# Optimization experiments

Hardware: AMD Instinct MI355X
Metric: run time of the kernel (lower is better)

## Reference

```python
import math
import jax, jax.numpy as jnp
import numpy as np


def _pairwise_sqdist(x, y):
    # x: [N, d], y: [M, d] -> [N, M]
    x2 = jnp.sum(x * x, axis=-1)[:, None]
    y2 = jnp.sum(y * y, axis=-1)[None, :]
    return jnp.maximum(x2 + y2 - 2.0 * (x @ y.T), 0.0)


def setup_inputs() -> dict:
    key = jax.random.key(0)
    k1, k2 = jax.random.split(key)
    N, M, D = 8192, 8192, 2
    base_points = jax.random.normal(k1, (N, D), dtype=jnp.float32)
    target_points = jax.random.normal(k2, (M, D), dtype=jnp.float32)
    log_sigma = jnp.asarray(math.log(0.1), dtype=jnp.float32)
    log_scale = jnp.zeros((D,), dtype=jnp.float32)
    return {
        "base_points": base_points,
        "target_points": target_points,
        "log_sigma": log_sigma,
        "log_scale": log_scale,
    }


def reference(base_points, target_points, log_sigma, log_scale):
    # learn_scale=True: anisotropic per-coordinate scaling
    scale = jnp.exp(log_scale)
    base = base_points * scale
    target = target_points * scale

    # uniform node weights (use_weight_net=False)
    N = base.shape[0]
    M = target.shape[0]
    w_base = jnp.full((N,), 1.0 / N, dtype=base.dtype)
    w_target = jnp.full((M,), 1.0 / M, dtype=target.dtype)

    # center=True: subtract weighted centroid of each cloud
    base = base - jnp.sum(w_base[:, None] * base, axis=0, keepdims=True)
    target = target - jnp.sum(w_target[:, None] * target, axis=0, keepdims=True)

    sigma = jnp.exp(log_sigma)
    inv2s2 = 1.0 / (2.0 * sigma * sigma)

    k_bb = jnp.exp(-_pairwise_sqdist(base, base) * inv2s2)      # [N, N]
    k_tt = jnp.exp(-_pairwise_sqdist(target, target) * inv2s2)  # [M, M]
    k_bt = jnp.exp(-_pairwise_sqdist(base, target) * inv2s2)    # [N, M]

    term_bb = w_base @ (k_bb @ w_base)
    term_tt = w_target @ (k_tt @ w_target)
    term_bt = w_base @ (k_bt @ w_target)
    loss = term_bb + term_tt - 2.0 * term_bt
    return loss
```

## Files before the change

kernel.cpp:

```cpp
#include <hip/hip_runtime.h>


#define BLOCK 256
#define NT_CROSS 1024
#define NT_TOT   2080
#define LOG2E 1.4426950408889634f

typedef float v2f __attribute__((ext_vector_type(2)));

struct Prep { float f0, f1, sh0, sh1; };

__device__ __forceinline__ float fexp2(float x) {
    return __builtin_amdgcn_exp2f(x);
}

__global__ __launch_bounds__(1024) void prep_kernel(
    const float* __restrict__ base, const float* __restrict__ target,
    const float* __restrict__ log_sigma, const float* __restrict__ log_scale,
    int N, int M, Prep* __restrict__ pp, double* __restrict__ slots)
{
    __shared__ double mred[16][4];
    const int tid = threadIdx.x;
    if (tid < 64) slots[tid] = 0.0;

    double sbx = 0, sby = 0, stx = 0, sty = 0;
    const float4* b4 = (const float4*)base;
    const float4* t4 = (const float4*)target;
    for (int i = tid; i < (N >> 1); i += 1024) {
        float4 v = b4[i];
        sbx += (double)v.x + (double)v.z;
        sby += (double)v.y + (double)v.w;
    }
    for (int i = tid; i < (M >> 1); i += 1024) {
        float4 v = t4[i];
        stx += (double)v.x + (double)v.z;
        sty += (double)v.y + (double)v.w;
    }
    for (int off = 32; off; off >>= 1) {
        sbx += __shfl_down(sbx, off); sby += __shfl_down(sby, off);
        stx += __shfl_down(stx, off); sty += __shfl_down(sty, off);
    }
    if ((tid & 63) == 0) {
        mred[tid >> 6][0] = sbx; mred[tid >> 6][1] = sby;
        mred[tid >> 6][2] = stx; mred[tid >> 6][3] = sty;
    }
    __syncthreads();
    if (tid == 0) {
        double b0 = 0, b1 = 0, t0 = 0, t1 = 0;
        for (int k = 0; k < 16; ++k) {
            b0 += mred[k][0]; b1 += mred[k][1];
            t0 += mred[k][2]; t1 += mred[k][3];
        }
        float s0 = expf(log_scale[0]);
        float s1 = expf(log_scale[1]);
        float sigma = expf(log_sigma[0]);
        float inv2s2 = 1.0f / (2.0f * sigma * sigma);
        float sq = sqrtf(inv2s2 * LOG2E);
        float f0 = s0 * sq, f1 = s1 * sq;
        pp->f0 = f0; pp->f1 = f1;
        pp->sh0 = (float)(b0 / (double)N - t0 / (double)M) * f0;
        pp->sh1 = (float)(b1 / (double)N - t1 / (double)M) * f1;
    }
}

__global__ __launch_bounds__(BLOCK, 8) void mmd_main(
    const float* __restrict__ base, const float* __restrict__ target,
    int N, int M, const Prep* __restrict__ pp, double* __restrict__ slots)
{
    __shared__ __align__(16) float tbx[256];
    __shared__ __align__(16) float tby[256];
    __shared__ __align__(16) float tbc[256];
    __shared__ double wredd[4];

    const int tid = threadIdx.x;
    const int t   = blockIdx.x;
    const Prep p = *pp;
    const float2* base2   = (const float2*)base;
    const float2* target2 = (const float2*)target;

    const double wNN = 1.0 / ((double)N * (double)N);
    const double wMM = 1.0 / ((double)M * (double)M);
    const double wNM = -2.0 / ((double)N * (double)M);

    int ib, jb, term;
    bool diag;
    const float2* A2;
    const float2* B2;
    double wt;
    float shx = 0.f, shy = 0.f;
    if (t < NT_CROSS) {
        ib = t >> 5; jb = t & 31;
        A2 = base2; B2 = target2;
        wt = wNM; diag = false; term = 2;
        shx = p.sh0; shy = p.sh1;
    } else {
        const int u = t - NT_CROSS;
        term = (u >= 528) ? 1 : 0;
        const int v = u - term * 528;
        int r = (int)((65.0f - sqrtf(4225.0f - 8.0f * (float)v)) * 0.5f);
        r = min(max(r, 0), 31);
        while (r > 0 && (r * (65 - r)) / 2 > v) --r;
        while (r < 31 && ((r + 1) * (64 - r)) / 2 <= v) ++r;
        ib = r;
        jb = r + (v - (r * (65 - r)) / 2);
        diag = (jb == ib);
        A2 = term ? target2 : base2;  B2 = A2;
        wt = 2.0 * (term ? wMM : wNN);
    }
    const int i0 = ib * 256, j0 = jb * 256;

    {
        float2 b = B2[j0 + tid];
        float bx = b.x * p.f0, by = b.y * p.f1;
        tbx[tid] = bx;
        tby[tid] = by;
        tbc[tid] = -fmaf(bx, bx, by * by);
    }
    __syncthreads();

    const int r0 = i0 + (tid & 127);
    const int js = (tid >> 7) * 128;

    float ax2s[2], ay2s[2], A0s[2];
#pragma unroll
    for (int k = 0; k < 2; ++k) {
        float2 a = A2[r0 + 128 * k];
        float ax = fmaf(a.x, p.f0, -shx);
        float ay = fmaf(a.y, p.f1, -shy);
        ax2s[k] = ax + ax;
        ay2s[k] = ay + ay;
        A0s[k]  = -fmaf(ax, ax, ay * ay);
    }

    const float4* bx4 = (const float4*)(tbx + js);
    const float4* by4 = (const float4*)(tby + js);
    const float4* c4  = (const float4*)(tbc + js);

    double result;
    if (!diag) {
        v2f s00 = {0.f, 0.f}, s01 = {0.f, 0.f};
        v2f s10 = {0.f, 0.f}, s11 = {0.f, 0.f};
#pragma unroll 4
        for (int q = 0; q < 32; ++q) {
            float4 BX = bx4[q];
            float4 BY = by4[q];
            float4 C  = c4[q];
            v2f bxa = { BX.x, BX.y }, bxb = { BX.z, BX.w };
            v2f bya = { BY.x, BY.y }, byb = { BY.z, BY.w };
            v2f ca  = { C.x,  C.y  }, cb  = { C.z,  C.w  };
            {
                v2f A0v = { A0s[0], A0s[0] };
                v2f axv = { ax2s[0], ax2s[0] };
                v2f ayv = { ay2s[0], ay2s[0] };
                v2f ea = axv * bxa + (ayv * bya + (ca + A0v));
                v2f eb = axv * bxb + (ayv * byb + (cb + A0v));
                s00 += (v2f){ fexp2(ea.x), fexp2(ea.y) };
                s01 += (v2f){ fexp2(eb.x), fexp2(eb.y) };
            }
            {
                v2f A0v = { A0s[1], A0s[1] };
                v2f axv = { ax2s[1], ax2s[1] };
                v2f ayv = { ay2s[1], ay2s[1] };
                v2f ea = axv * bxa + (ayv * bya + (ca + A0v));
                v2f eb = axv * bxb + (ayv * byb + (cb + A0v));
                s10 += (v2f){ fexp2(ea.x), fexp2(ea.y) };
                s11 += (v2f){ fexp2(eb.x), fexp2(eb.y) };
            }
        }
        v2f st0 = s00 + s01;
        v2f st1 = s10 + s11;
        result = wt * ((double)(st0.x + st0.y) + (double)(st1.x + st1.y));
    } else {
        float sge = 0.f, sgt = 0.f;
        const int jbase = j0 + js;
#pragma unroll 2
        for (int q = 0; q < 32; ++q) {
            float4 BX = bx4[q];
            float4 BY = by4[q];
            float4 C  = c4[q];
            const int j = jbase + 4 * q;
#pragma unroll
            for (int k = 0; k < 2; ++k) {
                const int row = r0 + 128 * k;
                float e0 = fmaf(ax2s[k], BX.x, fmaf(ay2s[k], BY.x, C.x + A0s[k]));
                float e1 = fmaf(ax2s[k], BX.y, fmaf(ay2s[k], BY.y, C.y + A0s[k]));
                float e2 = fmaf(ax2s[k], BX.z, fmaf(ay2s[k], BY.z, C.z + A0s[k]));
                float e3 = fmaf(ax2s[k], BX.w, fmaf(ay2s[k], BY.w, C.w + A0s[k]));
                float v0 = fexp2(e0), v1 = fexp2(e1);
                float v2 = fexp2(e2), v3 = fexp2(e3);
                sge += (j + 0 >= row) ? v0 : 0.f;  sgt += (j + 0 > row) ? v0 : 0.f;
                sge += (j + 1 >= row) ? v1 : 0.f;  sgt += (j + 1 > row) ? v1 : 0.f;
                sge += (j + 2 >= row) ? v2 : 0.f;  sgt += (j + 2 > row) ? v2 : 0.f;
                sge += (j + 3 >= row) ? v3 : 0.f;  sgt += (j + 3 > row) ? v3 : 0.f;
            }
        }
        result = (term ? wMM : wNN) * (double)(sge + sgt);
    }

    for (int off = 32; off; off >>= 1) result += __shfl_down(result, off);
    if ((tid & 63) == 0) wredd[tid >> 6] = result;
    __syncthreads();
    if (tid == 0) {
        double s = wredd[0] + wredd[1] + wredd[2] + wredd[3];
        atomicAdd(&slots[t & 63], s);
    }
}

__global__ void final_kernel(const double* __restrict__ slots,
                             float* __restrict__ out)
{
    const int tid = threadIdx.x;
    double s = slots[tid];
    for (int off = 32; off; off >>= 1) s += __shfl_down(s, off);
    if (tid == 0) out[0] = (float)s;
}

extern "C" void kernel_launch(void* const* d_in, const int* in_sizes, int n_in,
                              void* d_out, int out_size, void* d_ws, size_t ws_size,
                              hipStream_t stream)
{
    const float* base      = (const float*)d_in[0];
    const float* target    = (const float*)d_in[1];
    const float* log_sigma = (const float*)d_in[2];
    const float* log_scale = (const float*)d_in[3];
    float* out = (float*)d_out;

    int N = in_sizes[0] / 2;
    int M = in_sizes[1] / 2;

    Prep*   pp    = (Prep*)d_ws;
    double* slots = (double*)((char*)d_ws + 64);

    prep_kernel<<<1, 1024, 0, stream>>>(base, target, log_sigma, log_scale,
                                        N, M, pp, slots);
    mmd_main<<<NT_TOT, BLOCK, 0, stream>>>(base, target, N, M, pp, slots);
    final_kernel<<<1, 64, 0, stream>>>(slots, out);
}
```

Baseline: 90.53 us.

## Bucket-sort points by x and skip Gaussian tile quads beyond cutoff

Adds a counting-sort kernel that bins scaled, centred points by x into 512 buckets and writes them out as SoA arrays with precomputed squared norms. The main kernel then computes per-wave row x-ranges and per-quad column x-ranges, and skips four-column groups whose x-distance exceeds a cutoff, where the kernel value falls below about 2^-40. Block indices are permuted to balance the now-uneven work, and the rows handled by each thread become adjacent pairs. This trades an extra serial two-block sort kernel and branch divergence for skipping most exp evaluations. Skipped terms are treated as zero, which approximates the exact result only to within a tiny error.

```diff
diff --git a/kernel.cpp b/kernel.cpp
--- a/kernel.cpp
+++ b/kernel.cpp
@@ -4,7 +4,11 @@
 #define BLOCK 256
 #define NT_CROSS 1024
 #define NT_TOT   2080
-#define LOG2E 1.4426950408889634f
+#define LOG2E  1.4426950408889634f
+#define NBUCK  512
+#define BXMIN  (-64.0f)
+#define BSCALE 4.0f
+#define CUT    6.32455532f
 
 typedef float v2f __attribute__((ext_vector_type(2)));
 
@@ -63,20 +67,74 @@
     }
 }
 
+__global__ __launch_bounds__(1024) void sort_kernel(
+    const float* __restrict__ base, const float* __restrict__ target,
+    int N, int M, const Prep* __restrict__ pp,
+    float* __restrict__ xsB, float* __restrict__ ysB, float* __restrict__ csB,
+    float* __restrict__ xsT, float* __restrict__ ysT, float* __restrict__ csT)
+{
+    __shared__ unsigned hist[NBUCK];
+    __shared__ unsigned pref[NBUCK];
+    __shared__ unsigned cnt[NBUCK];
+    const int tid = threadIdx.x;
+    const Prep p = *pp;
+    const bool isB = (blockIdx.x == 0);
+    const float2* src = (const float2*)(isB ? base : target);
+    const int n = isB ? N : M;
+    float* xs = isB ? xsB : xsT;
+    float* ys = isB ? ysB : ysT;
+    float* cs = isB ? csB : csT;
+    const float shx = isB ? p.sh0 : 0.f;
+    const float shy = isB ? p.sh1 : 0.f;
+
+    for (int i = tid; i < NBUCK; i += 1024) { hist[i] = 0u; cnt[i] = 0u; }
+    __syncthreads();
+    for (int i = tid; i < n; i += 1024) {
+        float2 a = src[i];
+        float x = fmaf(a.x, p.f0, -shx);
+        int b = (int)((x - BXMIN) * BSCALE);
+        b = min(max(b, 0), NBUCK - 1);
+        atomicAdd(&hist[b], 1u);
+    }
+    __syncthreads();
+    if (tid < NBUCK) pref[tid] = hist[tid];
+    __syncthreads();
+    for (int off = 1; off < NBUCK; off <<= 1) {
+        unsigned v = 0u;
+        if (tid < NBUCK && tid >= off) v = pref[tid - off];
+        __syncthreads();
+        if (tid < NBUCK) pref[tid] += v;
+        __syncthreads();
+    }
+    for (int i = tid; i < n; i += 1024) {
+        float2 a = src[i];
+        float x = fmaf(a.x, p.f0, -shx);
+        float y = fmaf(a.y, p.f1, -shy);
+        int b = (int)((x - BXMIN) * BSCALE);
+        b = min(max(b, 0), NBUCK - 1);
+        unsigned pos = pref[b] - hist[b] + atomicAdd(&cnt[b], 1u);
+        xs[pos] = x;
+        ys[pos] = y;
+        cs[pos] = -fmaf(x, x, y * y);
+    }
+}
+
 __global__ __launch_bounds__(BLOCK, 8) void mmd_main(
-    const float* __restrict__ base, const float* __restrict__ target,
-    int N, int M, const Prep* __restrict__ pp, double* __restrict__ slots)
+    int N, int M,
+    const float* __restrict__ xsB, const float* __restrict__ ysB,
+    const float* __restrict__ csB,
+    const float* __restrict__ xsT, const float* __restrict__ ysT,
+    const float* __restrict__ csT,
+    double* __restrict__ slots)
 {
     __shared__ __align__(16) float tbx[256];
     __shared__ __align__(16) float tby[256];
     __shared__ __align__(16) float tbc[256];
+    __shared__ __align__(8)  float2 qb[64];
     __shared__ double wredd[4];
 
     const int tid = threadIdx.x;
-    const int t   = blockIdx.x;
-    const Prep p = *pp;
-    const float2* base2   = (const float2*)base;
-    const float2* target2 = (const float2*)target;
+    const int t   = (int)(((long long)blockIdx.x * 997) % NT_TOT);
 
     const double wNN = 1.0 / ((double)N * (double)N);
     const double wMM = 1.0 / ((double)M * (double)M);
@@ -84,15 +142,14 @@
 
     int ib, jb, term;
     bool diag;
-    const float2* A2;
-    const float2* B2;
+    const float* xA; const float* yA; const float* cA;
+    const float* xB; const float* yB; const float* cB;
     double wt;
-    float shx = 0.f, shy = 0.f;
     if (t < NT_CROSS) {
         ib = t >> 5; jb = t & 31;
-        A2 = base2; B2 = target2;
+        xA = xsB; yA = ysB; cA = csB;
+        xB = xsT; yB = ysT; cB = csT;
         wt = wNM; diag = false; term = 2;
-        shx = p.sh0; shy = p.sh1;
     } else {
         const int u = t - NT_CROSS;
         term = (u >= 528) ? 1 : 0;
@@ -104,44 +161,57 @@
         ib = r;
         jb = r + (v - (r * (65 - r)) / 2);
         diag = (jb == ib);
-        A2 = term ? target2 : base2;  B2 = A2;
+        if (term) { xA = xsT; yA = ysT; cA = csT; }
+        else      { xA = xsB; yA = ysB; cA = csB; }
+        xB = xA; yB = yA; cB = cA;
         wt = 2.0 * (term ? wMM : wNN);
     }
     const int i0 = ib * 256, j0 = jb * 256;
 
-    {
-        float2 b = B2[j0 + tid];
-        float bx = b.x * p.f0, by = b.y * p.f1;
-        tbx[tid] = bx;
-        tby[tid] = by;
-        tbc[tid] = -fmaf(bx, bx, by * by);
-    }
-    __syncthreads();
-
-    const int r0 = i0 + (tid & 127);
-    const int js = (tid >> 7) * 128;
-
-    float ax2s[2], ay2s[2], A0s[2];
-#pragma unroll
-    for (int k = 0; k < 2; ++k) {
-        float2 a = A2[r0 + 128 * k];
-        float ax = fmaf(a.x, p.f0, -shx);
-        float ay = fmaf(a.y, p.f1, -shy);
-        ax2s[k] = ax + ax;
-        ay2s[k] = ay + ay;
-        A0s[k]  = -fmaf(ax, ax, ay * ay);
-    }
+    tbx[tid] = xB[j0 + tid];
+    tby[tid] = yB[j0 + tid];
+    tbc[tid] = cB[j0 + tid];
+    if (tid < 64) {
+        float4 q4 = ((const float4*)(xB + j0))[tid];
+        float qlo = fminf(fminf(q4.x, q4.y), fminf(q4.z, q4.w));
+        float qhi = fmaxf(fmaxf(q4.x, q4.y), fmaxf(q4.z, q4.w));
+        qb[tid] = make_float2(qlo, qhi);
+    }
+    __syncthreads();
+
+    const int u_  = tid & 127;
+    const int r0  = i0 + 2 * u_;
+    const int js  = (tid >> 7) * 128;
+
+    float2 xr = ((const float2*)xA)[r0 >> 1];
+    float2 yr = ((const float2*)yA)[r0 >> 1];
+    float2 cr = ((const float2*)cA)[r0 >> 1];
+    float ax2s[2] = { xr.x + xr.x, xr.y + xr.y };
+    float ay2s[2] = { yr.x + yr.x, yr.y + yr.y };
+    float A0s[2]  = { cr.x, cr.y };
+
+    float rmin = fminf(xr.x, xr.y);
+    float rmax = fmaxf(xr.x, xr.y);
+    for (int off = 32; off; off >>= 1) {
+        rmin = fminf(rmin, __shfl_xor(rmin, off));
+        rmax = fmaxf(rmax, __shfl_xor(rmax, off));
+    }
+    const float rminc = rmin - CUT;
+    const float rmaxc = rmax + CUT;
 
     const float4* bx4 = (const float4*)(tbx + js);
     const float4* by4 = (const float4*)(tby + js);
     const float4* c4  = (const float4*)(tbc + js);
+    const int qoff = js >> 2;
 
     double result;
     if (!diag) {
         v2f s00 = {0.f, 0.f}, s01 = {0.f, 0.f};
         v2f s10 = {0.f, 0.f}, s11 = {0.f, 0.f};
-#pragma unroll 4
+#pragma unroll 2
         for (int q = 0; q < 32; ++q) {
+            float2 qr = qb[qoff + q];
+            if (qr.x > rmaxc || qr.y < rminc) continue;
             float4 BX = bx4[q];
             float4 BY = by4[q];
             float4 C  = c4[q];
@@ -175,13 +245,15 @@
         const int jbase = j0 + js;
 #pragma unroll 2
         for (int q = 0; q < 32; ++q) {
+            float2 qr = qb[qoff + q];
+            if (qr.x > rmaxc || qr.y < rminc) continue;
             float4 BX = bx4[q];
             float4 BY = by4[q];
             float4 C  = c4[q];
             const int j = jbase + 4 * q;
 #pragma unroll
             for (int k = 0; k < 2; ++k) {
-                const int row = r0 + 128 * k;
+                const int row = r0 + k;
                 float e0 = fmaf(ax2s[k], BX.x, fmaf(ay2s[k], BY.x, C.x + A0s[k]));
                 float e1 = fmaf(ax2s[k], BX.y, fmaf(ay2s[k], BY.y, C.y + A0s[k]));
                 float e2 = fmaf(ax2s[k], BX.z, fmaf(ay2s[k], BY.z, C.z + A0s[k]));
@@ -202,7 +274,7 @@
     __syncthreads();
     if (tid == 0) {
         double s = wredd[0] + wredd[1] + wredd[2] + wredd[3];
-        atomicAdd(&slots[t & 63], s);
+        atomicAdd(&slots[blockIdx.x & 63], s);
     }
 }
 
@@ -228,11 +300,22 @@
     int N = in_sizes[0] / 2;
     int M = in_sizes[1] / 2;
 
-    Prep*   pp    = (Prep*)d_ws;
-    double* slots = (double*)((char*)d_ws + 64);
+    char* ws = (char*)d_ws;
+    Prep*   pp    = (Prep*)ws;
+    double* slots = (double*)(ws + 256);
+    float*  arr   = (float*)(ws + 1024);
+    float* xsB = arr;
+    float* ysB = xsB + N;
+    float* csB = ysB + N;
+    float* xsT = csB + N;
+    float* ysT = xsT + M;
+    float* csT = ysT + M;
 
     prep_kernel<<<1, 1024, 0, stream>>>(base, target, log_sigma, log_scale,
                                         N, M, pp, slots);
-    mmd_main<<<NT_TOT, BLOCK, 0, stream>>>(base, target, N, M, pp, slots);
+    sort_kernel<<<2, 1024, 0, stream>>>(base, target, N, M, pp,
+                                        xsB, ysB, csB, xsT, ysT, csT);
+    mmd_main<<<NT_TOT, BLOCK, 0, stream>>>(N, M, xsB, ysB, csB,
+                                           xsT, ysT, csT, slots);
     final_kernel<<<1, 64, 0, stream>>>(slots, out);
 }
```

After: 102.1 us. +12.7%, slower.
